# Kernel tuning notes

Measured on AMD Instinct MI355X. Metric: run time of the kernel, lower is better.

Reference implementation:

```python
import jax, jax.numpy as jnp
import numpy as np

B, O, R = 4, 1000, 20000
NF, RD, ED = 6, 1, 100
RH, OH = 150, 100


def setup_inputs() -> dict:
    key = jax.random.key(0)
    ks = jax.random.split(key, 20)
    s = 0.05
    inp = {
        "objects": jax.random.normal(ks[0], (B, O, NF), jnp.float32),
        "sender_relations": jax.random.uniform(ks[1], (B, O, R), jnp.float32),
        "receiver_relations": jax.random.uniform(ks[2], (B, O, R), jnp.float32),
        "relation_info": jax.random.normal(ks[3], (B, R, RD), jnp.float32),
        # relational MLP: (2*NF+RD) -> 150 -> 150 -> 150 -> ED, ReLU after every layer
        "rw1": jax.random.normal(ks[4], (2 * NF + RD, RH), jnp.float32) * s,
        "rb1": jnp.zeros((RH,), jnp.float32),
        "rw2": jax.random.normal(ks[5], (RH, RH), jnp.float32) * s,
        "rb2": jnp.zeros((RH,), jnp.float32),
        "rw3": jax.random.normal(ks[6], (RH, RH), jnp.float32) * s,
        "rb3": jnp.zeros((RH,), jnp.float32),
        "rw4": jax.random.normal(ks[7], (RH, ED), jnp.float32) * s,
        "rb4": jnp.zeros((ED,), jnp.float32),
        # object MLP: (NF+ED) -> 100 -> 2, ReLU only after first layer
        "ow1": jax.random.normal(ks[8], (NF + ED, OH), jnp.float32) * s,
        "ob1": jnp.zeros((OH,), jnp.float32),
        "ow2": jax.random.normal(ks[9], (OH, 2), jnp.float32) * s,
        "ob2": jnp.zeros((2,), jnp.float32),
    }
    return inp


def reference(objects, sender_relations, receiver_relations, relation_info,
              rw1, rb1, rw2, rb2, rw3, rb3, rw4, rb4,
              ow1, ob1, ow2, ob2):
    # marshalling: dense one-hot gather via bmm
    senders = jnp.einsum('bnr,bnf->brf', sender_relations, objects)    # [B,R,NF]
    receivers = jnp.einsum('bnr,bnf->brf', receiver_relations, objects)  # [B,R,NF]
    Bm = jnp.concatenate([senders, receivers, relation_info], axis=2)  # [B,R,2NF+RD]
    # relational MLP (ReLU after every layer, including the last)
    h = jax.nn.relu(Bm @ rw1 + rb1)
    h = jax.nn.relu(h @ rw2 + rb2)
    h = jax.nn.relu(h @ rw3 + rb3)
    E = jax.nn.relu(h @ rw4 + rb4)                                     # [B,R,ED]
    # aggregator: dense scatter via bmm
    effect_receivers = jnp.einsum('bnr,brf->bnf', receiver_relations, E)  # [B,O,ED]
    C = jnp.concatenate([objects, effect_receivers], axis=2)           # [B,O,NF+ED]
    # object MLP, flattened over batch*objects like the torch view(-1, input)
    Cf = C.reshape(-1, C.shape[-1])
    o = jax.nn.relu(Cf @ ow1 + ob1)
    return o @ ow2 + ob2                                               # [B*O, 2]
```

## Files before the change

kernel.cpp:

```cpp
#include <hip/hip_runtime.h>

#define B_   4
#define O_   1000
#define R_   20000
#define NF_  6
#define EDP_ 128
#define KS_  25
#define CHUNK_ 800
#define MPAD_ 1024

#define ET_OFF   2560000
#define PART_OFF 7680000
#define WT_USHORTS (4 * 2 * 25600)

typedef short bf16x8 __attribute__((ext_vector_type(8)));
typedef float f32x4  __attribute__((ext_vector_type(4)));
typedef unsigned short ushort4v __attribute__((ext_vector_type(4)));
typedef unsigned short ushort8v __attribute__((ext_vector_type(8)));

#define MFMA16 __builtin_amdgcn_mfma_f32_16x16x32_bf16

__device__ __forceinline__ unsigned short f2bf(float x) {
    union { float f; unsigned int u; } v; v.f = x;
    unsigned int r = (v.u + 0x7FFFu + ((v.u >> 16) & 1u)) >> 16;
    return (unsigned short)r;
}

__device__ __forceinline__ float bf2f(unsigned short h) {
    union { unsigned int u; float f; } v; v.u = (unsigned int)h << 16;
    return v.f;
}

__global__ __launch_bounds__(256) void k_prep(
    const float* __restrict__ rw1, const float* __restrict__ rb1,
    const float* __restrict__ rw2, const float* __restrict__ rb2,
    const float* __restrict__ rw3, const float* __restrict__ rb3,
    const float* __restrict__ rw4, const float* __restrict__ rb4,
    unsigned short* __restrict__ Wt, float* __restrict__ bfp)
{
    const int l = blockIdx.y;
    const float* Ws[4] = {rw1, rw2, rw3, rw4};
    const float* Bs[4] = {rb1, rb2, rb3, rb4};
    const int   Ksz[4] = {13, 150, 150, 150};
    const int   Nsz[4] = {150, 150, 150, 100};
    const float* w = Ws[l];
    const int K = Ksz[l], N = Nsz[l];

    int idx = blockIdx.x * 256 + threadIdx.x;
    if (idx < 25600) {
        int n = idx / 160, k = idx % 160;
        float v = (k < K && n < N) ? w[k * N + n] : 0.f;
        unsigned short h = f2bf(v);
        unsigned short lo = f2bf(v - bf2f(h));
        Wt[(size_t)l * 51200 + idx]         = h;
        Wt[(size_t)l * 51200 + 25600 + idx] = lo;
    }
    if (blockIdx.x == 0 && threadIdx.x < 160)
        bfp[l * 160 + threadIdx.x] = (threadIdx.x < (unsigned)N) ? Bs[l][threadIdx.x] : 0.f;
}

__global__ __launch_bounds__(256) void k_marshal(
    const float* __restrict__ obj, const float* __restrict__ S,
    const float* __restrict__ RRm, const float* __restrict__ rinfo,
    float* __restrict__ bmp)
{
    __shared__ float sobj[500 * NF_];
    const int b = blockIdx.y, z = blockIdx.z;
    const int n0 = z * 500;
    for (int i = threadIdx.x; i < 500 * NF_; i += 256)
        sobj[i] = obj[(size_t)b * O_ * NF_ + (size_t)n0 * NF_ + i];
    __syncthreads();

    const int r = blockIdx.x * 256 + threadIdx.x;
    if (r >= R_) return;

    const size_t base = (size_t)b * O_ * R_ + (size_t)n0 * R_ + r;
    const float* Sp = S + base;
    const float* Rp = RRm + base;

    float ss[NF_] = {0.f, 0.f, 0.f, 0.f, 0.f, 0.f};
    float rs[NF_] = {0.f, 0.f, 0.f, 0.f, 0.f, 0.f};

    #pragma unroll 4
    for (int n = 0; n < 500; ++n) {
        float sv = Sp[(size_t)n * R_];
        float rv = Rp[(size_t)n * R_];
        #pragma unroll
        for (int f = 0; f < NF_; ++f) {
            float o = sobj[n * NF_ + f];
            ss[f] = fmaf(sv, o, ss[f]);
            rs[f] = fmaf(rv, o, rs[f]);
        }
    }

    float* outp = bmp + ((size_t)z * 80000 + (size_t)b * R_ + r) * 16;
    #pragma unroll
    for (int f = 0; f < NF_; ++f) {
        outp[f]     = ss[f];
        outp[6 + f] = rs[f];
    }
    outp[12] = (z == 0) ? rinfo[(size_t)b * R_ + r] : 0.f;
}

template<int NT>
__device__ __forceinline__ void layer_mmW(
    const unsigned short (*act)[168],
    const unsigned short* __restrict__ Wh, const unsigned short* __restrict__ Wl,
    int arow0, int koff, int cl, int nb, f32x4 (*acc)[5])
{
    #pragma unroll
    for (int m = 0; m < 2; ++m)
        #pragma unroll
        for (int j = 0; j < NT; ++j) acc[m][j] = (f32x4){0.f, 0.f, 0.f, 0.f};
    #pragma unroll
    for (int ks = 0; ks < 5; ++ks) {
        bf16x8 a0 = *(const bf16x8*)&act[arow0][ks * 32 + koff];
        bf16x8 a1 = *(const bf16x8*)&act[arow0 + 16][ks * 32 + koff];
        #pragma unroll
        for (int j = 0; j < NT; ++j) {
            const size_t wo = (size_t)((nb + j) * 16 + cl) * 160 + ks * 32 + koff;
            bf16x8 wh = *(const bf16x8*)(Wh + wo);
            bf16x8 wl = *(const bf16x8*)(Wl + wo);
            acc[0][j] = MFMA16(a0, wh, acc[0][j], 0, 0, 0);
            acc[0][j] = MFMA16(a0, wl, acc[0][j], 0, 0, 0);
            acc[1][j] = MFMA16(a1, wh, acc[1][j], 0, 0, 0);
            acc[1][j] = MFMA16(a1, wl, acc[1][j], 0, 0, 0);
        }
    }
}

template<int NT>
__device__ __forceinline__ void epiW(
    f32x4 (*acc)[5], const float* __restrict__ bias,
    unsigned short (*out)[168], int m0, int cl, int rg0, int nb)
{
    #pragma unroll
    for (int m = 0; m < 2; ++m) {
        #pragma unroll
        for (int j = 0; j < NT; ++j) {
            int col = (nb + j) * 16 + cl;
            float bv = bias[col];
            #pragma unroll
            for (int rg = 0; rg < 4; ++rg) {
                float v = fmaxf(acc[m][j][rg] + bv, 0.f);
                out[m0 + m * 16 + rg0 + rg][col] = f2bf(v);
            }
        }
    }
}

__global__ __launch_bounds__(256) void k_mlp(
    const float* __restrict__ bmp, unsigned short* __restrict__ Et,
    const unsigned short* __restrict__ Wt, const float* __restrict__ bfp)
{
    __shared__ unsigned short act[64][168];
    __shared__ unsigned short alo[64][32];
    const int t = threadIdx.x;
    const size_t row0 = (size_t)blockIdx.x * 64;

    for (int idx = t; idx < 64 * 32; idx += 256) {
        int rr = idx >> 5, k = idx & 31;
        float v = 0.f;
        if (k < 13)
            v = bmp[(row0 + rr) * 16 + k]
              + bmp[(size_t)80000 * 16 + (row0 + rr) * 16 + k];
        unsigned short h = f2bf(v);
        act[rr][k] = h;
        alo[rr][k] = f2bf(v - bf2f(h));
    }
    __syncthreads();

    const int lane = t & 63, wave = t >> 6;
    const int wm = wave >> 1, wn = wave & 1;
    const int m0    = wm * 32;
    const int arow0 = m0 + (lane & 15);
    const int koff  = (lane >> 4) * 8;
    const int cl    = lane & 15;
    const int rg0   = (lane >> 4) * 4;

    f32x4 acc[2][5];

    {
        const unsigned short* Wh = Wt;
        const unsigned short* Wl = Wt + 25600;
        bf16x8 ah0 = *(const bf16x8*)&act[arow0][koff];
        bf16x8 al0 = *(const bf16x8*)&alo[arow0][koff];
        bf16x8 ah1 = *(const bf16x8*)&act[arow0 + 16][koff];
        bf16x8 al1 = *(const bf16x8*)&alo[arow0 + 16][koff];
        #pragma unroll
        for (int j = 0; j < 5; ++j) {
            const size_t wo = (size_t)((wn * 5 + j) * 16 + cl) * 160 + koff;
            bf16x8 wh = *(const bf16x8*)(Wh + wo);
            bf16x8 wl = *(const bf16x8*)(Wl + wo);
            f32x4 a = (f32x4){0.f, 0.f, 0.f, 0.f};
            a = MFMA16(ah0, wh, a, 0, 0, 0);
            a = MFMA16(ah0, wl, a, 0, 0, 0);
            a = MFMA16(al0, wh, a, 0, 0, 0);
            acc[0][j] = a;
            f32x4 c = (f32x4){0.f, 0.f, 0.f, 0.f};
            c = MFMA16(ah1, wh, c, 0, 0, 0);
            c = MFMA16(ah1, wl, c, 0, 0, 0);
            c = MFMA16(al1, wh, c, 0, 0, 0);
            acc[1][j] = c;
        }
    }
    __syncthreads();
    epiW<5>(acc, bfp + 0 * 160, act, m0, cl, rg0, wn * 5);
    __syncthreads();

    layer_mmW<5>(act, Wt + 1 * 51200, Wt + 1 * 51200 + 25600, arow0, koff, cl, wn * 5, acc);
    __syncthreads();
    epiW<5>(acc, bfp + 1 * 160, act, m0, cl, rg0, wn * 5);
    __syncthreads();

    layer_mmW<5>(act, Wt + 2 * 51200, Wt + 2 * 51200 + 25600, arow0, koff, cl, wn * 5, acc);
    __syncthreads();
    epiW<5>(acc, bfp + 2 * 160, act, m0, cl, rg0, wn * 5);
    __syncthreads();

    if (wn == 0)
        layer_mmW<4>(act, Wt + 3 * 51200, Wt + 3 * 51200 + 25600, arow0, koff, cl, 0, acc);
    else
        layer_mmW<3>(act, Wt + 3 * 51200, Wt + 3 * 51200 + 25600, arow0, koff, cl, 4, acc);
    __syncthreads();
    if (wn == 0)
        epiW<4>(acc, bfp + 3 * 160, act, m0, cl, rg0, 0);
    else
        epiW<3>(acc, bfp + 3 * 160, act, m0, cl, rg0, 4);
    __syncthreads();

    for (int idx = t; idx < 64 * 128; idx += 256) {
        int rr = idx & 63, j = idx >> 6;
        size_t gr = row0 + rr;
        int b = (int)(gr / R_);
        int r = (int)(gr - (size_t)b * R_);
        Et[((size_t)(b * EDP_ + j)) * R_ + r] = (j < 100) ? act[rr][j] : (unsigned short)0;
    }
}

__global__ __launch_bounds__(256) void k_agg(
    const float* __restrict__ RRm, const unsigned short* __restrict__ Et,
    float* __restrict__ part)
{
    __shared__ unsigned short sB[2][128][36];
    const int t = threadIdx.x;
    const int mt = blockIdx.x, b = blockIdx.y, kz = blockIdx.z;
    const int lane = t & 63, wave = t >> 6;
    const int k0 = kz * CHUNK_;

    const int br0 = t >> 2, bc0 = (t & 3) * 8;
    const int br1 = br0 + 64;
    const unsigned short* EtB = Et + (size_t)b * EDP_ * R_;

    const int cl = lane & 15, koff = (lane >> 4) * 8;
    int n0 = mt * 128 + wave * 32 + cl;
    int n1 = n0 + 16;
    if (n0 > 999) n0 = 999;
    if (n1 > 999) n1 = 999;
    const float* Ap0 = RRm + ((size_t)(b * O_) + n0) * R_ + k0 + koff;
    const float* Ap1 = RRm + ((size_t)(b * O_) + n1) * R_ + k0 + koff;

    f32x4 acc[2][8] = {};
    float4 a0c, a1c, a2c, a3c;
    float4 a0n = {0,0,0,0}, a1n = {0,0,0,0}, a2n = {0,0,0,0}, a3n = {0,0,0,0};

    {
        ushort8v v0 = *(const ushort8v*)(EtB + (size_t)br0 * R_ + k0 + bc0);
        ushort8v v1 = *(const ushort8v*)(EtB + (size_t)br1 * R_ + k0 + bc0);
        *(ushort8v*)&sB[0][br0][bc0] = v0;
        *(ushort8v*)&sB[0][br1][bc0] = v1;
        a0c = *(const float4*)(Ap0 + 0);
        a1c = *(const float4*)(Ap0 + 4);
        a2c = *(const float4*)(Ap1 + 0);
        a3c = *(const float4*)(Ap1 + 4);
    }
    __syncthreads();

    for (int it = 0; it < CHUNK_ / 32; ++it) {
        const int cur = it & 1, nxt = cur ^ 1;
        const bool more = (it + 1 < CHUNK_ / 32);
        ushort8v v0, v1;
        if (more) {
            const int kb = k0 + (it + 1) * 32;
            v0 = *(const ushort8v*)(EtB + (size_t)br0 * R_ + kb + bc0);
            v1 = *(const ushort8v*)(EtB + (size_t)br1 * R_ + kb + bc0);
            a0n = *(const float4*)(Ap0 + (it + 1) * 32);
            a1n = *(const float4*)(Ap0 + (it + 1) * 32 + 4);
            a2n = *(const float4*)(Ap1 + (it + 1) * 32);
            a3n = *(const float4*)(Ap1 + (it + 1) * 32 + 4);
        }
        bf16x8 af0, af1;
        af0[0] = (short)f2bf(a0c.x); af0[1] = (short)f2bf(a0c.y);
        af0[2] = (short)f2bf(a0c.z); af0[3] = (short)f2bf(a0c.w);
        af0[4] = (short)f2bf(a1c.x); af0[5] = (short)f2bf(a1c.y);
        af0[6] = (short)f2bf(a1c.z); af0[7] = (short)f2bf(a1c.w);
        af1[0] = (short)f2bf(a2c.x); af1[1] = (short)f2bf(a2c.y);
        af1[2] = (short)f2bf(a2c.z); af1[3] = (short)f2bf(a2c.w);
        af1[4] = (short)f2bf(a3c.x); af1[5] = (short)f2bf(a3c.y);
        af1[6] = (short)f2bf(a3c.z); af1[7] = (short)f2bf(a3c.w);
        #pragma unroll
        for (int ni = 0; ni < 8; ++ni) {
            bf16x8 bf = *(const bf16x8*)&sB[cur][ni * 16 + cl][koff];
            acc[0][ni] = MFMA16(af0, bf, acc[0][ni], 0, 0, 0);
            acc[1][ni] = MFMA16(af1, bf, acc[1][ni], 0, 0, 0);
        }
        if (more) {
            *(ushort8v*)&sB[nxt][br0][bc0] = v0;
            *(ushort8v*)&sB[nxt][br1][bc0] = v1;
        }
        __syncthreads();
        a0c = a0n; a1c = a1n; a2c = a2n; a3c = a3n;
    }

    float* pp = part + ((size_t)(kz * 4 + b) * MPAD_) * 128;
    #pragma unroll
    for (int mg = 0; mg < 2; ++mg) {
        const int rowb = mt * 128 + wave * 32 + mg * 16 + (lane >> 4) * 4;
        #pragma unroll
        for (int ni = 0; ni < 8; ++ni)
            #pragma unroll
            for (int rg = 0; rg < 4; ++rg)
                pp[(size_t)(rowb + rg) * 128 + ni * 16 + cl] = acc[mg][ni][rg];
    }
}

__global__ __launch_bounds__(256) void k_obj(
    const float* __restrict__ obj, const float* __restrict__ part,
    const float* __restrict__ ow1, const float* __restrict__ ob1,
    const float* __restrict__ ow2, const float* __restrict__ ob2,
    float* __restrict__ out)
{
    __shared__ float C[8][112];
    __shared__ float h[8][104];
    const int t = threadIdx.x;
    const int g0 = blockIdx.x * 8;

    for (int idx = t; idx < 8 * NF_; idx += 256) {
        int rr = idx / NF_, f = idx % NF_;
        C[rr][f] = obj[(size_t)(g0 + rr) * NF_ + f];
    }
    for (int idx = t; idx < 8 * 100; idx += 256) {
        int rr = idx / 100, f = idx % 100;
        int g = g0 + rr, b = g / 1000, n = g % 1000;
        float s = 0.f;
        for (int z = 0; z < KS_; ++z)
            s += part[((size_t)(z * 4 + b) * MPAD_ + n) * 128 + f];
        C[rr][6 + f] = s;
    }
    __syncthreads();

    for (int idx = t; idx < 8 * 100; idx += 256) {
        int rr = idx / 100, j = idx % 100;
        float acc = ob1[j];
        for (int k = 0; k < 106; ++k)
            acc = fmaf(C[rr][k], ow1[k * 100 + j], acc);
        h[rr][j] = fmaxf(acc, 0.f);
    }
    __syncthreads();

    if (t < 16) {
        int rr = t >> 1, j = t & 1;
        float acc = ob2[j];
        for (int k = 0; k < 100; ++k)
            acc = fmaf(h[rr][k], ow2[k * 2 + j], acc);
        out[(size_t)(g0 + rr) * 2 + j] = acc;
    }
}

extern "C" void kernel_launch(void* const* d_in, const int* in_sizes, int n_in,
                              void* d_out, int out_size, void* d_ws, size_t ws_size,
                              hipStream_t stream)
{
    const float* obj   = (const float*)d_in[0];
    const float* S     = (const float*)d_in[1];
    const float* RRm   = (const float*)d_in[2];
    const float* rinfo = (const float*)d_in[3];
    const float* rw1   = (const float*)d_in[4];
    const float* rb1   = (const float*)d_in[5];
    const float* rw2   = (const float*)d_in[6];
    const float* rb2   = (const float*)d_in[7];
    const float* rw3   = (const float*)d_in[8];
    const float* rb3   = (const float*)d_in[9];
    const float* rw4   = (const float*)d_in[10];
    const float* rb4   = (const float*)d_in[11];
    const float* ow1   = (const float*)d_in[12];
    const float* ob1   = (const float*)d_in[13];
    const float* ow2   = (const float*)d_in[14];
    const float* ob2   = (const float*)d_in[15];

    float* ws            = (float*)d_ws;
    float* bmp           = ws;
    unsigned short* Et   = (unsigned short*)(ws + ET_OFF);
    float* part          = ws + PART_OFF;
    unsigned short* Wt   = (unsigned short*)(ws + PART_OFF);
    float* bfp           = ws + PART_OFF + (WT_USHORTS / 2);
    float* out           = (float*)d_out;

    k_prep<<<dim3(100, 4), 256, 0, stream>>>(rw1, rb1, rw2, rb2, rw3, rb3, rw4, rb4,
                                             Wt, bfp);
    k_marshal<<<dim3(79, 4, 2), 256, 0, stream>>>(obj, S, RRm, rinfo, bmp);
    k_mlp<<<dim3(1250), 256, 0, stream>>>(bmp, Et, Wt, bfp);
    k_agg<<<dim3(8, 4, KS_), 256, 0, stream>>>(RRm, Et, part);
    k_obj<<<dim3(500), 256, 0, stream>>>(obj, part, ow1, ob1, ow2, ob2, out);
}
```

Before: 354.6 us.

## Retile relational MLP to 128-row blocks with 8 waves, 64 rows per wave

Each k_mlp block now handles 128 relation rows with 512 threads. Each wave covers 64 rows (four 16-row MFMA tiles) and fewer output column tiles (3/3/2/2 of 10, then 2/2/2/1 for the last layer). The aim is to reuse each weight fragment loaded from global memory across more rows, cutting weight traffic per row. The cost is more accumulator registers per thread and half as many blocks (625), which may reduce occupancy or load balance.

```diff
diff --git a/kernel.cpp b/kernel.cpp
--- a/kernel.cpp
+++ b/kernel.cpp
@@ -103,19 +103,21 @@
 }
 
 template<int NT>
-__device__ __forceinline__ void layer_mmW(
+__device__ __forceinline__ void layer_mm4(
     const unsigned short (*act)[168],
     const unsigned short* __restrict__ Wh, const unsigned short* __restrict__ Wl,
-    int arow0, int koff, int cl, int nb, f32x4 (*acc)[5])
-{
-    #pragma unroll
-    for (int m = 0; m < 2; ++m)
+    int arow0, int koff, int cl, int nb, f32x4 (*acc)[3])
+{
+    #pragma unroll
+    for (int m = 0; m < 4; ++m)
         #pragma unroll
         for (int j = 0; j < NT; ++j) acc[m][j] = (f32x4){0.f, 0.f, 0.f, 0.f};
     #pragma unroll
     for (int ks = 0; ks < 5; ++ks) {
-        bf16x8 a0 = *(const bf16x8*)&act[arow0][ks * 32 + koff];
+        bf16x8 a0 = *(const bf16x8*)&act[arow0 +  0][ks * 32 + koff];
         bf16x8 a1 = *(const bf16x8*)&act[arow0 + 16][ks * 32 + koff];
+        bf16x8 a2 = *(const bf16x8*)&act[arow0 + 32][ks * 32 + koff];
+        bf16x8 a3 = *(const bf16x8*)&act[arow0 + 48][ks * 32 + koff];
         #pragma unroll
         for (int j = 0; j < NT; ++j) {
             const size_t wo = (size_t)((nb + j) * 16 + cl) * 160 + ks * 32 + koff;
@@ -125,17 +127,58 @@
             acc[0][j] = MFMA16(a0, wl, acc[0][j], 0, 0, 0);
             acc[1][j] = MFMA16(a1, wh, acc[1][j], 0, 0, 0);
             acc[1][j] = MFMA16(a1, wl, acc[1][j], 0, 0, 0);
+            acc[2][j] = MFMA16(a2, wh, acc[2][j], 0, 0, 0);
+            acc[2][j] = MFMA16(a2, wl, acc[2][j], 0, 0, 0);
+            acc[3][j] = MFMA16(a3, wh, acc[3][j], 0, 0, 0);
+            acc[3][j] = MFMA16(a3, wl, acc[3][j], 0, 0, 0);
         }
     }
 }
 
 template<int NT>
-__device__ __forceinline__ void epiW(
-    f32x4 (*acc)[5], const float* __restrict__ bias,
+__device__ __forceinline__ void l1_mm4(
+    const unsigned short (*act)[168], const unsigned short (*alo)[32],
+    const unsigned short* __restrict__ Wt,
+    int arow0, int koff, int cl, int nb, f32x4 (*acc)[3])
+{
+    const unsigned short* Wh = Wt;
+    const unsigned short* Wl = Wt + 25600;
+    bf16x8 ah0 = *(const bf16x8*)&act[arow0 +  0][koff];
+    bf16x8 ah1 = *(const bf16x8*)&act[arow0 + 16][koff];
+    bf16x8 ah2 = *(const bf16x8*)&act[arow0 + 32][koff];
+    bf16x8 ah3 = *(const bf16x8*)&act[arow0 + 48][koff];
+    bf16x8 al0 = *(const bf16x8*)&alo[arow0 +  0][koff];
+    bf16x8 al1 = *(const bf16x8*)&alo[arow0 + 16][koff];
+    bf16x8 al2 = *(const bf16x8*)&alo[arow0 + 32][koff];
+    bf16x8 al3 = *(const bf16x8*)&alo[arow0 + 48][koff];
+    #pragma unroll
+    for (int j = 0; j < NT; ++j) {
+        const size_t wo = (size_t)((nb + j) * 16 + cl) * 160 + koff;
+        bf16x8 wh = *(const bf16x8*)(Wh + wo);
+        bf16x8 wl = *(const bf16x8*)(Wl + wo);
+        f32x4 a;
+        a = (f32x4){0.f, 0.f, 0.f, 0.f};
+        a = MFMA16(ah0, wh, a, 0, 0, 0); a = MFMA16(ah0, wl, a, 0, 0, 0);
+        a = MFMA16(al0, wh, a, 0, 0, 0); acc[0][j] = a;
+        a = (f32x4){0.f, 0.f, 0.f, 0.f};
+        a = MFMA16(ah1, wh, a, 0, 0, 0); a = MFMA16(ah1, wl, a, 0, 0, 0);
+        a = MFMA16(al1, wh, a, 0, 0, 0); acc[1][j] = a;
+        a = (f32x4){0.f, 0.f, 0.f, 0.f};
+        a = MFMA16(ah2, wh, a, 0, 0, 0); a = MFMA16(ah2, wl, a, 0, 0, 0);
+        a = MFMA16(al2, wh, a, 0, 0, 0); acc[2][j] = a;
+        a = (f32x4){0.f, 0.f, 0.f, 0.f};
+        a = MFMA16(ah3, wh, a, 0, 0, 0); a = MFMA16(ah3, wl, a, 0, 0, 0);
+        a = MFMA16(al3, wh, a, 0, 0, 0); acc[3][j] = a;
+    }
+}
+
+template<int NT>
+__device__ __forceinline__ void epi4(
+    f32x4 (*acc)[3], const float* __restrict__ bias,
     unsigned short (*out)[168], int m0, int cl, int rg0, int nb)
 {
     #pragma unroll
-    for (int m = 0; m < 2; ++m) {
+    for (int m = 0; m < 4; ++m) {
         #pragma unroll
         for (int j = 0; j < NT; ++j) {
             int col = (nb + j) * 16 + cl;
@@ -149,16 +192,16 @@
     }
 }
 
-__global__ __launch_bounds__(256) void k_mlp(
+__global__ __launch_bounds__(512) void k_mlp(
     const float* __restrict__ bmp, unsigned short* __restrict__ Et,
     const unsigned short* __restrict__ Wt, const float* __restrict__ bfp)
 {
-    __shared__ unsigned short act[64][168];
-    __shared__ unsigned short alo[64][32];
+    __shared__ unsigned short act[128][168];
+    __shared__ unsigned short alo[128][32];
     const int t = threadIdx.x;
-    const size_t row0 = (size_t)blockIdx.x * 64;
-
-    for (int idx = t; idx < 64 * 32; idx += 256) {
+    const size_t row0 = (size_t)blockIdx.x * 128;
+
+    for (int idx = t; idx < 128 * 32; idx += 512) {
         int rr = idx >> 5, k = idx & 31;
         float v = 0.f;
         if (k < 13)
@@ -171,66 +214,50 @@
     __syncthreads();
 
     const int lane = t & 63, wave = t >> 6;
-    const int wm = wave >> 1, wn = wave & 1;
-    const int m0    = wm * 32;
+    const int wm = wave >> 2, wn = wave & 3;
+    const int m0    = wm * 64;
     const int arow0 = m0 + (lane & 15);
     const int koff  = (lane >> 4) * 8;
     const int cl    = lane & 15;
     const int rg0   = (lane >> 4) * 4;
 
-    f32x4 acc[2][5];
-
-    {
-        const unsigned short* Wh = Wt;
-        const unsigned short* Wl = Wt + 25600;
-        bf16x8 ah0 = *(const bf16x8*)&act[arow0][koff];
-        bf16x8 al0 = *(const bf16x8*)&alo[arow0][koff];
-        bf16x8 ah1 = *(const bf16x8*)&act[arow0 + 16][koff];
-        bf16x8 al1 = *(const bf16x8*)&alo[arow0 + 16][koff];
-        #pragma unroll
-        for (int j = 0; j < 5; ++j) {
-            const size_t wo = (size_t)((wn * 5 + j) * 16 + cl) * 160 + koff;
-            bf16x8 wh = *(const bf16x8*)(Wh + wo);
-            bf16x8 wl = *(const bf16x8*)(Wl + wo);
-            f32x4 a = (f32x4){0.f, 0.f, 0.f, 0.f};
-            a = MFMA16(ah0, wh, a, 0, 0, 0);
-            a = MFMA16(ah0, wl, a, 0, 0, 0);
-            a = MFMA16(al0, wh, a, 0, 0, 0);
-            acc[0][j] = a;
-            f32x4 c = (f32x4){0.f, 0.f, 0.f, 0.f};
-            c = MFMA16(ah1, wh, c, 0, 0, 0);
-            c = MFMA16(ah1, wl, c, 0, 0, 0);
-            c = MFMA16(al1, wh, c, 0, 0, 0);
-            acc[1][j] = c;
-        }
-    }
-    __syncthreads();
-    epiW<5>(acc, bfp + 0 * 160, act, m0, cl, rg0, wn * 5);
-    __syncthreads();
-
-    layer_mmW<5>(act, Wt + 1 * 51200, Wt + 1 * 51200 + 25600, arow0, koff, cl, wn * 5, acc);
-    __syncthreads();
-    epiW<5>(acc, bfp + 1 * 160, act, m0, cl, rg0, wn * 5);
-    __syncthreads();
-
-    layer_mmW<5>(act, Wt + 2 * 51200, Wt + 2 * 51200 + 25600, arow0, koff, cl, wn * 5, acc);
-    __syncthreads();
-    epiW<5>(acc, bfp + 2 * 160, act, m0, cl, rg0, wn * 5);
-    __syncthreads();
-
-    if (wn == 0)
-        layer_mmW<4>(act, Wt + 3 * 51200, Wt + 3 * 51200 + 25600, arow0, koff, cl, 0, acc);
-    else
-        layer_mmW<3>(act, Wt + 3 * 51200, Wt + 3 * 51200 + 25600, arow0, koff, cl, 4, acc);
-    __syncthreads();
-    if (wn == 0)
-        epiW<4>(acc, bfp + 3 * 160, act, m0, cl, rg0, 0);
-    else
-        epiW<3>(acc, bfp + 3 * 160, act, m0, cl, rg0, 4);
-    __syncthreads();
-
-    for (int idx = t; idx < 64 * 128; idx += 256) {
-        int rr = idx & 63, j = idx >> 6;
+    const int NB123[4] = {0, 3, 6, 8};
+    const int NB4[4]   = {0, 2, 4, 6};
+    const int nb123 = NB123[wn];
+    const int nb4   = NB4[wn];
+
+    f32x4 acc[4][3];
+
+    if (wn < 2) l1_mm4<3>(act, alo, Wt, arow0, koff, cl, nb123, acc);
+    else        l1_mm4<2>(act, alo, Wt, arow0, koff, cl, nb123, acc);
+    __syncthreads();
+    if (wn < 2) epi4<3>(acc, bfp + 0 * 160, act, m0, cl, rg0, nb123);
+    else        epi4<2>(acc, bfp + 0 * 160, act, m0, cl, rg0, nb123);
+    __syncthreads();
+
+    if (wn < 2) layer_mm4<3>(act, Wt + 1 * 51200, Wt + 1 * 51200 + 25600, arow0, koff, cl, nb123, acc);
+    else        layer_mm4<2>(act, Wt + 1 * 51200, Wt + 1 * 51200 + 25600, arow0, koff, cl, nb123, acc);
+    __syncthreads();
+    if (wn < 2) epi4<3>(acc, bfp + 1 * 160, act, m0, cl, rg0, nb123);
+    else        epi4<2>(acc, bfp + 1 * 160, act, m0, cl, rg0, nb123);
+    __syncthreads();
+
+    if (wn < 2) layer_mm4<3>(act, Wt + 2 * 51200, Wt + 2 * 51200 + 25600, arow0, koff, cl, nb123, acc);
+    else        layer_mm4<2>(act, Wt + 2 * 51200, Wt + 2 * 51200 + 25600, arow0, koff, cl, nb123, acc);
+    __syncthreads();
+    if (wn < 2) epi4<3>(acc, bfp + 2 * 160, act, m0, cl, rg0, nb123);
+    else        epi4<2>(acc, bfp + 2 * 160, act, m0, cl, rg0, nb123);
+    __syncthreads();
+
+    if (wn < 3) layer_mm4<2>(act, Wt + 3 * 51200, Wt + 3 * 51200 + 25600, arow0, koff, cl, nb4, acc);
+    else        layer_mm4<1>(act, Wt + 3 * 51200, Wt + 3 * 51200 + 25600, arow0, koff, cl, nb4, acc);
+    __syncthreads();
+    if (wn < 3) epi4<2>(acc, bfp + 3 * 160, act, m0, cl, rg0, nb4);
+    else        epi4<1>(acc, bfp + 3 * 160, act, m0, cl, rg0, nb4);
+    __syncthreads();
+
+    for (int idx = t; idx < 128 * 128; idx += 512) {
+        int rr = idx & 127, j = idx >> 7;
         size_t gr = row0 + rr;
         int b = (int)(gr / R_);
         int r = (int)(gr - (size_t)b * R_);
@@ -399,7 +426,7 @@
     k_prep<<<dim3(100, 4), 256, 0, stream>>>(rw1, rb1, rw2, rb2, rw3, rb3, rw4, rb4,
                                              Wt, bfp);
     k_marshal<<<dim3(79, 4, 2), 256, 0, stream>>>(obj, S, RRm, rinfo, bmp);
-    k_mlp<<<dim3(1250), 256, 0, stream>>>(bmp, Et, Wt, bfp);
+    k_mlp<<<dim3(625), 512, 0, stream>>>(bmp, Et, Wt, bfp);
     k_agg<<<dim3(8, 4, KS_), 256, 0, stream>>>(RRm, Et, part);
     k_obj<<<dim3(500), 256, 0, stream>>>(obj, part, ow1, ob1, ow2, ob2, out);
 }
```

After: 339.2 us. -4.3%, faster.
